# Performance work log

Measured on AMD Instinct MI355X. Metric: run time of the kernel, lower is better.

The kernel has to match this reference:

```python
import jax, jax.numpy as jnp
import numpy as np

N_NODES = 20000
NUM_DRUGS = 2048
NUM_DPI = 200000
IN_C = 256
EMB = 256
HID = 512
OUT = 1
N_CL = 8
B = 16384


def setup_inputs() -> dict:
    key = jax.random.key(0)
    ks = jax.random.split(key, 10)
    x = jax.random.normal(ks[0], (N_NODES, IN_C), jnp.float32)
    # bipartite DPI edges: drug ids in [0, NUM_DRUGS), protein ids in [NUM_DRUGS, N_NODES)
    d = jax.random.randint(ks[1], (NUM_DPI,), 0, NUM_DRUGS)
    p = jax.random.randint(ks[2], (NUM_DPI,), NUM_DRUGS, N_NODES)
    edge_index = jnp.concatenate([jnp.stack([d, p]), jnp.stack([p, d])], axis=1)  # [2, 2*NUM_DPI]
    drug_drug_batch = jax.random.randint(ks[3], (2, B), 0, NUM_DRUGS)
    edge_cell_lines = jax.random.randint(ks[4], (B,), 0, N_CL)
    Wg1 = jax.random.normal(ks[5], (IN_C, EMB), jnp.float32) / np.float32(np.sqrt(IN_C))
    bg1 = jnp.zeros((EMB,), jnp.float32)
    Wg2 = jax.random.normal(ks[6], (EMB, EMB), jnp.float32) / np.float32(np.sqrt(EMB))
    bg2 = jnp.zeros((EMB,), jnp.float32)
    W1 = jax.random.normal(ks[7], (N_CL, 2 * EMB, HID), jnp.float32) / np.float32(np.sqrt(2 * EMB))
    b1 = jnp.zeros((N_CL, HID), jnp.float32)
    W2 = jax.random.normal(ks[8], (N_CL, HID, OUT), jnp.float32) / np.float32(np.sqrt(HID))
    b2 = jnp.zeros((N_CL, OUT), jnp.float32)
    return dict(x=x, edge_index=edge_index, drug_drug_batch=drug_drug_batch,
                edge_cell_lines=edge_cell_lines, num_drugs=NUM_DRUGS,
                Wg1=Wg1, bg1=bg1, Wg2=Wg2, bg2=bg2, W1=W1, b1=b1, W2=W2, b2=b2)


def _gcn(h_in, row, col, W, b, n):
    # PyG GCNConv: self-loops already appended to (row, col); symmetric normalization.
    h = h_in @ W  # [N, EMB]
    deg = jax.ops.segment_sum(jnp.ones(col.shape[0], h.dtype), col, num_segments=n)
    dinv = jnp.where(deg > 0, jax.lax.rsqrt(jnp.maximum(deg, 1e-12)), 0.0)
    msg = h[row] * (dinv[row] * dinv[col])[:, None]
    return jax.ops.segment_sum(msg, col, num_segments=n) + b


def reference(x, edge_index, drug_drug_batch, edge_cell_lines, num_drugs,
              Wg1, bg1, Wg2, bg2, W1, b1, W2, b2):
    n = x.shape[0]
    ar = jnp.arange(n, dtype=edge_index.dtype)
    row = jnp.concatenate([edge_index[0], ar])
    col = jnp.concatenate([edge_index[1], ar])
    h = jax.nn.relu(_gcn(x, row, col, Wg1, bg1, n))
    h = jax.nn.relu(_gcn(h, row, col, Wg2, bg2, n))
    # scatter-mean pool node embeddings of proteins into per-drug graph embeddings
    num_dpi = edge_index.shape[1] // 2
    avg = jnp.sort(edge_index[:, :num_dpi], axis=0)  # row0=drug id, row1=protein id
    node_emb = h[avg[1]]  # [NUM_DPI, EMB]
    sums = jax.ops.segment_sum(node_emb, avg[0], num_segments=num_drugs)
    cnt = jax.ops.segment_sum(jnp.ones(num_dpi, h.dtype), avg[0], num_segments=num_drugs)
    graph = sums / jnp.maximum(cnt, 1.0)[:, None]  # [NUM_DRUGS, EMB]
    xcat = jnp.concatenate([graph[drug_drug_batch[0]], graph[drug_drug_batch[1]]], axis=1)  # [B, 2*EMB]
    # per-cell-line MLP routing: run each expert over all rows, then gather per-row expert output
    n_cl = W1.shape[0]
    outs = jnp.stack([jax.nn.relu(xcat @ W1[c] + b1[c]) @ W2[c] + b2[c] for c in range(n_cl)])  # [C, B, OUT]
    preds = outs[edge_cell_lines, jnp.arange(xcat.shape[0])]  # [B, OUT]
    return preds
```

## Files before the change

### kernel.cpp

```cpp
#include <hip/hip_runtime.h>
#include <hip/hip_bf16.h>

#define N_NODES 20000
#define NUM_DRUGS 2048
#define N_PROT (N_NODES - NUM_DRUGS)
#define NUM_DPI 200000
#define E2 400000
#define CDIM 256
#define HID 512
#define N_CL 8
#define BATCH 16384
#define HN 8192

#define STRD 32
#define STRP 16
#define ELLD 192
#define ELLP 48

#define NB_T64 512
#define NB_TWG 32
#define NB_ZERO 79
#define NB_SPLIT 20000

#define MT_NODE 313

#define NB_AGG_D NUM_DRUGS
#define NB_AGG_P ((N_PROT + 3) / 4)

typedef __attribute__((ext_vector_type(8))) short short8;
typedef __attribute__((ext_vector_type(4))) float floatx4;

__device__ inline unsigned short f2bf(float f) {
    unsigned u = __float_as_uint(f);
    u += 0x7fff + ((u >> 16) & 1);
    return (unsigned short)(u >> 16);
}
__device__ inline float bf2f(unsigned short h) {
    return __uint_as_float((unsigned)h << 16);
}
__device__ inline void split2(float v, unsigned short& h, unsigned short& l) {
    h = f2bf(v);
    l = f2bf(v - bf2f(h));
}
__device__ inline void gload16(const void* g, void* l) {
    __builtin_amdgcn_global_load_lds(
        (const __attribute__((address_space(1))) void*)g,
        (__attribute__((address_space(3))) void*)l, 16, 0, 0);
}
__device__ inline float4 f4fma(float4 v, float s, float4 a) {
    a.x = fmaf(v.x, s, a.x); a.y = fmaf(v.y, s, a.y);
    a.z = fmaf(v.z, s, a.z); a.w = fmaf(v.w, s, a.w);
    return a;
}
__device__ inline float4 bf4(const unsigned short* p) {
    ushort4 q = *(const ushort4*)p;
    return make_float4(bf2f(q.x), bf2f(q.y), bf2f(q.z), bf2f(q.w));
}

__global__ __launch_bounds__(256) void prep_all(
        const float* __restrict__ x, unsigned short* __restrict__ xhi,
        unsigned short* __restrict__ xlo,
        const float* __restrict__ Wg1, const float* __restrict__ Wg2,
        unsigned short* __restrict__ wg1Th, unsigned short* __restrict__ wg1Tl,
        unsigned short* __restrict__ wg2Th, unsigned short* __restrict__ wg2Tl,
        const float* __restrict__ W1, unsigned short* __restrict__ W1Th,
        unsigned short* __restrict__ W1Tl,
        int* __restrict__ cur_d, int* __restrict__ cur_p) {
    __shared__ float ld[64 * 65];
    int b = blockIdx.x;
    int t = threadIdx.x;
    int tx = t & 63, ty = t >> 6;
    if (b < NB_T64) {
        int m = b >> 5;
        int k0 = (b & 3) * 64, n0 = ((b >> 2) & 7) * 64;
        const float* Wm = W1 + (size_t)m * CDIM * HID;
#pragma unroll
        for (int rr = 0; rr < 16; rr++) {
            int kl = rr * 4 + ty;
            ld[tx * 65 + kl] = Wm[(size_t)(k0 + kl) * HID + n0 + tx];
        }
        __syncthreads();
        size_t obase = (size_t)m * HID * CDIM;
#pragma unroll
        for (int rr = 0; rr < 16; rr++) {
            int nl = rr * 4 + ty;
            float v = ld[nl * 65 + tx];
            unsigned short h, l;
            split2(v, h, l);
            size_t o = obase + (size_t)(n0 + nl) * CDIM + k0 + tx;
            W1Th[o] = h;
            W1Tl[o] = l;
        }
        return;
    }
    b -= NB_T64;
    if (b < NB_TWG) {
        const float* W = (b >> 4) ? Wg2 : Wg1;
        unsigned short* hi = (b >> 4) ? wg2Th : wg1Th;
        unsigned short* lo = (b >> 4) ? wg2Tl : wg1Tl;
        int k0 = (b & 3) * 64, n0 = ((b >> 2) & 3) * 64;
#pragma unroll
        for (int rr = 0; rr < 16; rr++) {
            int kl = rr * 4 + ty;
            ld[tx * 65 + kl] = W[(size_t)(k0 + kl) * CDIM + n0 + tx];
        }
        __syncthreads();
#pragma unroll
        for (int rr = 0; rr < 16; rr++) {
            int nl = rr * 4 + ty;
            float v = ld[nl * 65 + tx];
            unsigned short h, l;
            split2(v, h, l);
            size_t o = (size_t)(n0 + nl) * CDIM + k0 + tx;
            hi[o] = h;
            lo[o] = l;
        }
        return;
    }
    b -= NB_TWG;
    if (b < NB_ZERO) {
        int i = b * 256 + t;
        if (i < N_NODES) cur_p[i * STRP] = 0;
        if (i < NUM_DRUGS) cur_d[i * STRD] = 0;
        return;
    }
    b -= NB_ZERO;
    {
        int i = b * 256 + t;
        unsigned short h, l;
        split2(x[i], h, l);
        xhi[i] = h;
        xlo[i] = l;
    }
}

__global__ void fill_ell(const int* __restrict__ ei, int* cur_d, int* adj_drug,
                         int* cur_p, int* adj_prot) {
    int e = blockIdx.x * blockDim.x + threadIdx.x;
    if (e >= NUM_DPI) return;
    int d = ei[e];
    int p = ei[E2 + e];
    int posd = atomicAdd(&cur_d[d * STRD], 1);
    int posp = atomicAdd(&cur_p[p * STRP], 1);
    if (posd < ELLD) adj_drug[d * ELLD + posd] = p;
    if (posp < ELLP) adj_prot[(size_t)p * ELLP + posp] = d;
}

template <int BM, int SWZ>
__global__ __launch_bounds__(256) void gemm_mfma(
        const unsigned short* __restrict__ Ahi, const unsigned short* __restrict__ Alo,
        const unsigned short* __restrict__ BThi, const unsigned short* __restrict__ BTlo,
        float* __restrict__ C, unsigned short* __restrict__ Cbf,
        int M, int K, int N, int mTiles,
        const int* __restrict__ cur_d, const int* __restrict__ cur_p,
        float* __restrict__ dinv) {
    if ((int)blockIdx.x >= mTiles) {
        int i = (((int)blockIdx.x - mTiles) * (int)gridDim.y + (int)blockIdx.y) * 256
                + (int)threadIdx.x;
        if (i < N_NODES) {
            int deg = (i < NUM_DRUGS) ? cur_d[i * STRD] : cur_p[i * STRP];
            dinv[i] = rsqrtf((float)(deg + 1));
        }
        return;
    }
    constexpr int MI = BM / 32;
    __shared__ unsigned short sAh[2][BM * 32], sAl[2][BM * 32];
    __shared__ unsigned short sBh[2][4096], sBl[2][4096];
    int t = threadIdx.x;
    int wv = t >> 6, lane = t & 63, quad = lane >> 4, l15 = lane & 15;
    int bx = blockIdx.x, by = blockIdx.y;
    if constexpr (SWZ) {
        int w = by * 16 + bx;
        bx = (w >> 3) & 15;
        by = ((w >> 7) << 3) | (w & 7);
    }
    int m0 = bx * BM, n0 = by * 128;
    int m0w = (wv >> 1) * (BM / 2), n0w = (wv & 1) * 64;
    floatx4 zero = {0.f, 0.f, 0.f, 0.f};
    floatx4 acc[MI][4];
#pragma unroll
    for (int i = 0; i < MI; i++)
#pragma unroll
        for (int j = 0; j < 4; j++) acc[i][j] = zero;

    auto STAGE = [&](int buf, int kk) {
#pragma unroll
        for (int s = t; s < BM * 4; s += 256) {
            int row = s >> 2, pos = s & 3;
            int ch = pos ^ ((row >> 1) & 3);
            int arow = m0 + row; if (arow > M - 1) arow = M - 1;
            size_t aoff = (size_t)arow * K + kk + ch * 8;
            gload16(Ahi + aoff, &sAh[buf][s * 8]);
            gload16(Alo + aoff, &sAl[buf][s * 8]);
        }
#pragma unroll
        for (int s = t; s < 512; s += 256) {
            int row = s >> 2, pos = s & 3;
            int ch = pos ^ ((row >> 1) & 3);
            int brow = n0 + row; if (brow > N - 1) brow = N - 1;
            size_t boff = (size_t)brow * K + kk + ch * 8;
            gload16(BThi + boff, &sBh[buf][s * 8]);
            gload16(BTlo + boff, &sBl[buf][s * 8]);
        }
    };

    int nk = K >> 5;
    STAGE(0, 0);
    asm volatile("s_waitcnt vmcnt(0)" ::: "memory");
    __builtin_amdgcn_s_barrier();
    int cur = 0;
    for (int it = 0; it < nk; ++it) {
        if (it + 1 < nk) STAGE(cur ^ 1, (it + 1) << 5);
        short8 ah[MI], al[MI], bh[4], bl[4];
        int posq = quad ^ ((l15 >> 1) & 3);
#pragma unroll
        for (int i = 0; i < MI; i++) {
            int sl = (m0w + i * 16 + l15) * 4 + posq;
            ah[i] = *(const short8*)&sAh[cur][sl * 8];
            al[i] = *(const short8*)&sAl[cur][sl * 8];
        }
#pragma unroll
        for (int j = 0; j < 4; j++) {
            int sl = (n0w + j * 16 + l15) * 4 + posq;
            bh[j] = *(const short8*)&sBh[cur][sl * 8];
            bl[j] = *(const short8*)&sBl[cur][sl * 8];
        }
#pragma unroll
        for (int i = 0; i < MI; i++)
#pragma unroll
            for (int j = 0; j < 4; j++) {
                acc[i][j] = __builtin_amdgcn_mfma_f32_16x16x32_bf16(ah[i], bh[j], acc[i][j], 0, 0, 0);
                acc[i][j] = __builtin_amdgcn_mfma_f32_16x16x32_bf16(ah[i], bl[j], acc[i][j], 0, 0, 0);
                acc[i][j] = __builtin_amdgcn_mfma_f32_16x16x32_bf16(al[i], bh[j], acc[i][j], 0, 0, 0);
            }
        if (it + 1 < nk) {
            asm volatile("s_waitcnt vmcnt(0)" ::: "memory");
            __builtin_amdgcn_s_barrier();
            cur ^= 1;
        }
    }
#pragma unroll
    for (int i = 0; i < MI; i++) {
        int gr = m0 + m0w + i * 16 + quad * 4;
#pragma unroll
        for (int r = 0; r < 4; r++) {
            if (gr + r < M) {
#pragma unroll
                for (int j = 0; j < 4; j++) {
                    size_t o = (size_t)(gr + r) * N + n0 + n0w + j * 16 + l15;
                    float v = acc[i][j][r];
                    if (C) C[o] = v;
                    if (Cbf) Cbf[o] = f2bf(v);
                }
            }
        }
    }
}

__global__ __launch_bounds__(256) void aggregate1(const float* __restrict__ tmp,
                                                  const unsigned short* __restrict__ tmpbf,
                                                  const int* __restrict__ cur_d,
                                                  const int* __restrict__ adj_drug,
                                                  const int* __restrict__ cur_p,
                                                  const int* __restrict__ adj_prot,
                                                  const float* __restrict__ dinv,
                                                  const float* __restrict__ bias,
                                                  unsigned short* __restrict__ outhi,
                                                  unsigned short* __restrict__ outlo) {
    __shared__ float4 red[4][64];
    int b = blockIdx.x;
    int lane = threadIdx.x & 63;
    if (b < NB_AGG_D) {
        int d = b;
        int w = threadIdx.x >> 6;
        const int* adj = adj_drug + (size_t)d * ELLD;
        int ecnt = cur_d[d * STRD];
        int e = ecnt < ELLD ? ecnt : ELLD;
        float4 a0 = make_float4(0.f, 0.f, 0.f, 0.f);
        float4 a1 = a0, a2 = a0, a3 = a0;
        int idx = w;
        for (; idx + 12 < e; idx += 16) {
            int j0 = adj[idx], j1 = adj[idx + 4], j2 = adj[idx + 8], j3 = adj[idx + 12];
            float d0 = dinv[j0], d1 = dinv[j1], d2 = dinv[j2], d3 = dinv[j3];
            float4 v0 = bf4(&tmpbf[(size_t)j0 * CDIM + lane * 4]);
            float4 v1 = bf4(&tmpbf[(size_t)j1 * CDIM + lane * 4]);
            float4 v2 = bf4(&tmpbf[(size_t)j2 * CDIM + lane * 4]);
            float4 v3 = bf4(&tmpbf[(size_t)j3 * CDIM + lane * 4]);
            a0 = f4fma(v0, d0, a0);
            a1 = f4fma(v1, d1, a1);
            a2 = f4fma(v2, d2, a2);
            a3 = f4fma(v3, d3, a3);
        }
        for (; idx < e; idx += 4) {
            int j = adj[idx];
            a0 = f4fma(bf4(&tmpbf[(size_t)j * CDIM + lane * 4]), dinv[j], a0);
        }
        a0.x = (a0.x + a1.x) + (a2.x + a3.x);
        a0.y = (a0.y + a1.y) + (a2.y + a3.y);
        a0.z = (a0.z + a1.z) + (a2.z + a3.z);
        a0.w = (a0.w + a1.w) + (a2.w + a3.w);
        red[w][lane] = a0;
        __syncthreads();
        if (w == 0) {
            float di = dinv[d];
            float4 r0 = red[0][lane], r1 = red[1][lane], r2 = red[2][lane], r3 = red[3][lane];
            float4 self = ((const float4*)(tmp + (size_t)d * CDIM))[lane];
            float4 acc;
            acc.x = (r0.x + r1.x) + (r2.x + r3.x) + self.x * di;
            acc.y = (r0.y + r1.y) + (r2.y + r3.y) + self.y * di;
            acc.z = (r0.z + r1.z) + (r2.z + r3.z) + self.z * di;
            acc.w = (r0.w + r1.w) + (r2.w + r3.w) + self.w * di;
            float4 bv = ((const float4*)bias)[lane];
            float4 r;
            r.x = fmaxf(fmaf(acc.x, di, bv.x), 0.f);
            r.y = fmaxf(fmaf(acc.y, di, bv.y), 0.f);
            r.z = fmaxf(fmaf(acc.z, di, bv.z), 0.f);
            r.w = fmaxf(fmaf(acc.w, di, bv.w), 0.f);
            ushort4 h, l;
            split2(r.x, h.x, l.x); split2(r.y, h.y, l.y);
            split2(r.z, h.z, l.z); split2(r.w, h.w, l.w);
            *(ushort4*)&outhi[(size_t)d * CDIM + lane * 4] = h;
            *(ushort4*)&outlo[(size_t)d * CDIM + lane * 4] = l;
        }
        return;
    }
    int i = NUM_DRUGS + (b - NB_AGG_D) * 4 + (threadIdx.x >> 6);
    if (i >= N_NODES) return;
    float di = dinv[i];
    float4 a0 = make_float4(0.f, 0.f, 0.f, 0.f);
    float4 a1 = a0, a2 = a0, a3 = a0;
    const int* adj = adj_prot + (size_t)i * ELLP;
    int e = cur_p[i * STRP];
    int idx = 0;
    for (; idx + 4 <= e; idx += 4) {
        int j0 = adj[idx + 0], j1 = adj[idx + 1];
        int j2 = adj[idx + 2], j3 = adj[idx + 3];
        float d0 = dinv[j0], d1 = dinv[j1], d2 = dinv[j2], d3 = dinv[j3];
        float4 v0 = ((const float4*)(tmp + (size_t)j0 * CDIM))[lane];
        float4 v1 = ((const float4*)(tmp + (size_t)j1 * CDIM))[lane];
        float4 v2 = ((const float4*)(tmp + (size_t)j2 * CDIM))[lane];
        float4 v3 = ((const float4*)(tmp + (size_t)j3 * CDIM))[lane];
        a0 = f4fma(v0, d0, a0);
        a1 = f4fma(v1, d1, a1);
        a2 = f4fma(v2, d2, a2);
        a3 = f4fma(v3, d3, a3);
    }
    for (; idx < e; idx++) {
        int j = adj[idx];
        a0 = f4fma(((const float4*)(tmp + (size_t)j * CDIM))[lane], dinv[j], a0);
    }
    float4 self = ((const float4*)(tmp + (size_t)i * CDIM))[lane];
    float4 acc;
    acc.x = (a0.x + a1.x) + (a2.x + a3.x) + self.x * di;
    acc.y = (a0.y + a1.y) + (a2.y + a3.y) + self.y * di;
    acc.z = (a0.z + a1.z) + (a2.z + a3.z) + self.z * di;
    acc.w = (a0.w + a1.w) + (a2.w + a3.w) + self.w * di;
    float4 bv = ((const float4*)bias)[lane];
    float4 r;
    r.x = fmaxf(fmaf(acc.x, di, bv.x), 0.f);
    r.y = fmaxf(fmaf(acc.y, di, bv.y), 0.f);
    r.z = fmaxf(fmaf(acc.z, di, bv.z), 0.f);
    r.w = fmaxf(fmaf(acc.w, di, bv.w), 0.f);
    ushort4 h, l;
    split2(r.x, h.x, l.x); split2(r.y, h.y, l.y);
    split2(r.z, h.z, l.z); split2(r.w, h.w, l.w);
    *(ushort4*)&outhi[(size_t)i * CDIM + lane * 4] = h;
    *(ushort4*)&outlo[(size_t)i * CDIM + lane * 4] = l;
}

__global__ __launch_bounds__(256) void aggregate2p(const float* __restrict__ tmp2,
                                                   const int* __restrict__ cur_p,
                                                   const int* __restrict__ adj_prot,
                                                   const float* __restrict__ dinv,
                                                   const float* __restrict__ bias,
                                                   unsigned short* __restrict__ h2bf) {
    int w = (blockIdx.x * blockDim.x + threadIdx.x) >> 6;
    int lane = threadIdx.x & 63;
    if (w >= N_PROT) return;
    int i = NUM_DRUGS + w;
    float di = dinv[i];
    float4 a0 = make_float4(0.f, 0.f, 0.f, 0.f);
    float4 a1 = a0, a2 = a0, a3 = a0;
    const int* adj = adj_prot + (size_t)i * ELLP;
    int e = cur_p[i * STRP];
    int idx = 0;
    for (; idx + 4 <= e; idx += 4) {
        int j0 = adj[idx + 0], j1 = adj[idx + 1];
        int j2 = adj[idx + 2], j3 = adj[idx + 3];
        float d0 = dinv[j0], d1 = dinv[j1], d2 = dinv[j2], d3 = dinv[j3];
        float4 v0 = ((const float4*)(tmp2 + (size_t)j0 * CDIM))[lane];
        float4 v1 = ((const float4*)(tmp2 + (size_t)j1 * CDIM))[lane];
        float4 v2 = ((const float4*)(tmp2 + (size_t)j2 * CDIM))[lane];
        float4 v3 = ((const float4*)(tmp2 + (size_t)j3 * CDIM))[lane];
        a0 = f4fma(v0, d0, a0);
        a1 = f4fma(v1, d1, a1);
        a2 = f4fma(v2, d2, a2);
        a3 = f4fma(v3, d3, a3);
    }
    for (; idx < e; idx++) {
        int j = adj[idx];
        a0 = f4fma(((const float4*)(tmp2 + (size_t)j * CDIM))[lane], dinv[j], a0);
    }
    float4 self = ((const float4*)(tmp2 + (size_t)i * CDIM))[lane];
    float4 acc;
    acc.x = (a0.x + a1.x) + (a2.x + a3.x) + self.x * di;
    acc.y = (a0.y + a1.y) + (a2.y + a3.y) + self.y * di;
    acc.z = (a0.z + a1.z) + (a2.z + a3.z) + self.z * di;
    acc.w = (a0.w + a1.w) + (a2.w + a3.w) + self.w * di;
    float4 bv = ((const float4*)bias)[lane];
    ushort4 o;
    o.x = f2bf(fmaxf(fmaf(acc.x, di, bv.x), 0.f));
    o.y = f2bf(fmaxf(fmaf(acc.y, di, bv.y), 0.f));
    o.z = f2bf(fmaxf(fmaf(acc.z, di, bv.z), 0.f));
    o.w = f2bf(fmaxf(fmaf(acc.w, di, bv.w), 0.f));
    *(ushort4*)&h2bf[(size_t)i * CDIM + lane * 4] = o;
}

__global__ __launch_bounds__(256) void pool_drugs(const unsigned short* __restrict__ h2bf,
                                                  unsigned short* __restrict__ Ghi,
                                                  unsigned short* __restrict__ Glo,
                                                  const int* __restrict__ cur_d,
                                                  const int* __restrict__ adj_drug) {
    __shared__ float4 red[4][64];
    int d = blockIdx.x;
    int w = threadIdx.x >> 6, lane = threadIdx.x & 63;
    const int* adj = adj_drug + (size_t)d * ELLD;
    int ecnt = cur_d[d * STRD];
    int e = ecnt < ELLD ? ecnt : ELLD;
    float4 a0 = make_float4(0.f, 0.f, 0.f, 0.f);
    float4 a1 = a0, a2 = a0, a3 = a0;
    int idx = w;
    for (; idx + 12 < e; idx += 16) {
        int j0 = adj[idx], j1 = adj[idx + 4], j2 = adj[idx + 8], j3 = adj[idx + 12];
        float4 v0 = bf4(&h2bf[(size_t)j0 * CDIM + lane * 4]);
        float4 v1 = bf4(&h2bf[(size_t)j1 * CDIM + lane * 4]);
        float4 v2 = bf4(&h2bf[(size_t)j2 * CDIM + lane * 4]);
        float4 v3 = bf4(&h2bf[(size_t)j3 * CDIM + lane * 4]);
        a0.x += v0.x; a0.y += v0.y; a0.z += v0.z; a0.w += v0.w;
        a1.x += v1.x; a1.y += v1.y; a1.z += v1.z; a1.w += v1.w;
        a2.x += v2.x; a2.y += v2.y; a2.z += v2.z; a2.w += v2.w;
        a3.x += v3.x; a3.y += v3.y; a3.z += v3.z; a3.w += v3.w;
    }
    for (; idx < e; idx += 4) {
        float4 v = bf4(&h2bf[(size_t)adj[idx] * CDIM + lane * 4]);
        a0.x += v.x; a0.y += v.y; a0.z += v.z; a0.w += v.w;
    }
    a0.x = (a0.x + a1.x) + (a2.x + a3.x);
    a0.y = (a0.y + a1.y) + (a2.y + a3.y);
    a0.z = (a0.z + a1.z) + (a2.z + a3.z);
    a0.w = (a0.w + a1.w) + (a2.w + a3.w);
    red[w][lane] = a0;
    __syncthreads();
    if (w == 0) {
        float4 r0 = red[0][lane], r1 = red[1][lane], r2 = red[2][lane], r3 = red[3][lane];
        float4 acc;
        acc.x = (r0.x + r1.x) + (r2.x + r3.x);
        acc.y = (r0.y + r1.y) + (r2.y + r3.y);
        acc.z = (r0.z + r1.z) + (r2.z + r3.z);
        acc.w = (r0.w + r1.w) + (r2.w + r3.w);
        float sc = 1.f / (float)(ecnt > 1 ? ecnt : 1);
        acc.x *= sc; acc.y *= sc; acc.z *= sc; acc.w *= sc;
        ushort4 h, l;
        split2(acc.x, h.x, l.x); split2(acc.y, h.y, l.y);
        split2(acc.z, h.z, l.z); split2(acc.w, h.w, l.w);
        *(ushort4*)&Ghi[(size_t)d * CDIM + lane * 4] = h;
        *(ushort4*)&Glo[(size_t)d * CDIM + lane * 4] = l;
    }
}

__global__ __launch_bounds__(256) void mlp_out(const unsigned short* __restrict__ Hbf,
                                               const int* __restrict__ ddb,
                                               const int* __restrict__ ecl,
                                               const float* __restrict__ b1,
                                               const float* __restrict__ W2,
                                               const float* __restrict__ b2,
                                               float* __restrict__ outp) {
    int r = (blockIdx.x * blockDim.x + threadIdx.x) >> 6;
    int lane = threadIdx.x & 63;
    if (r >= BATCH) return;
    int c = ecl[r];
    int d0 = ddb[r], d1 = ddb[BATCH + r];
    int n = lane * 8;
    const unsigned short* h0 = Hbf + (size_t)d0 * HN + (size_t)(c * 2) * HID + n;
    const unsigned short* h1 = Hbf + (size_t)d1 * HN + (size_t)(c * 2 + 1) * HID + n;
    const float* b1e = b1 + (size_t)c * HID + n;
    const float* w2e = W2 + (size_t)c * HID + n;
    short8 a8 = *(const short8*)h0;
    short8 b8 = *(const short8*)h1;
    float4 bb0 = *(const float4*)(b1e);
    float4 bb1 = *(const float4*)(b1e + 4);
    float4 w0 = *(const float4*)(w2e);
    float4 w1 = *(const float4*)(w2e + 4);
    float s = 0.f;
    float h;
    h = bf2f((unsigned short)a8[0]) + bf2f((unsigned short)b8[0]) + bb0.x;
    s = fmaf(fmaxf(h, 0.f), w0.x, s);
    h = bf2f((unsigned short)a8[1]) + bf2f((unsigned short)b8[1]) + bb0.y;
    s = fmaf(fmaxf(h, 0.f), w0.y, s);
    h = bf2f((unsigned short)a8[2]) + bf2f((unsigned short)b8[2]) + bb0.z;
    s = fmaf(fmaxf(h, 0.f), w0.z, s);
    h = bf2f((unsigned short)a8[3]) + bf2f((unsigned short)b8[3]) + bb0.w;
    s = fmaf(fmaxf(h, 0.f), w0.w, s);
    h = bf2f((unsigned short)a8[4]) + bf2f((unsigned short)b8[4]) + bb1.x;
    s = fmaf(fmaxf(h, 0.f), w1.x, s);
    h = bf2f((unsigned short)a8[5]) + bf2f((unsigned short)b8[5]) + bb1.y;
    s = fmaf(fmaxf(h, 0.f), w1.y, s);
    h = bf2f((unsigned short)a8[6]) + bf2f((unsigned short)b8[6]) + bb1.z;
    s = fmaf(fmaxf(h, 0.f), w1.z, s);
    h = bf2f((unsigned short)a8[7]) + bf2f((unsigned short)b8[7]) + bb1.w;
    s = fmaf(fmaxf(h, 0.f), w1.w, s);
    s += __shfl_xor(s, 1);
    s += __shfl_xor(s, 2);
    s += __shfl_xor(s, 4);
    s += __shfl_xor(s, 8);
    s += __shfl_xor(s, 16);
    s += __shfl_xor(s, 32);
    if (lane == 0) outp[r] = s + b2[c];
}

extern "C" void kernel_launch(void* const* d_in, const int* in_sizes, int n_in,
                              void* d_out, int out_size, void* d_ws, size_t ws_size,
                              hipStream_t stream) {
    const float* x   = (const float*)d_in[0];
    const int* ei    = (const int*)d_in[1];
    const int* ddb   = (const int*)d_in[2];
    const int* ecl   = (const int*)d_in[3];
    const float* Wg1 = (const float*)d_in[5];
    const float* bg1 = (const float*)d_in[6];
    const float* Wg2 = (const float*)d_in[7];
    const float* bg2 = (const float*)d_in[8];
    const float* W1  = (const float*)d_in[9];
    const float* b1  = (const float*)d_in[10];
    const float* W2  = (const float*)d_in[11];
    const float* b2  = (const float*)d_in[12];
    float* outp = (float*)d_out;

    const size_t NC = (size_t)N_NODES * CDIM;
    const size_t HRES = (size_t)NUM_DRUGS * HN * sizeof(float);
    char* r0 = (char*)d_ws;
    unsigned short* Hbf   = (unsigned short*)d_ws;
    float* tmp            = (float*)r0;
    unsigned short* t1bf  = (unsigned short*)(r0 + 20480000);
    unsigned short* h2bf  = t1bf;
    unsigned short* h1hi  = (unsigned short*)(r0 + 30720000);
    unsigned short* h1lo  = (unsigned short*)(r0 + 40960000);
    unsigned short* xhi   = h1hi;
    unsigned short* xlo   = h1lo;
    char* p = r0 + 51200000;
    auto alloc = [&](size_t bytes) {
        char* r = p;
        p += (bytes + 255) & ~size_t(255);
        return (void*)r;
    };
    float* dinv    = (float*)alloc(sizeof(float) * N_NODES);
    int* cur_d     = (int*)alloc(sizeof(int) * NUM_DRUGS * STRD);
    int* cur_p     = (int*)alloc(sizeof(int) * N_NODES * STRP);
    int* adj_drug  = (int*)alloc(sizeof(int) * NUM_DRUGS * ELLD);
    int* adj_prot  = (int*)alloc(sizeof(int) * (size_t)N_NODES * ELLP);
    p = (char*)d_ws + ((HRES + 255) & ~size_t(255));
    unsigned short* Ghi   = (unsigned short*)alloc(2 * NUM_DRUGS * CDIM);
    unsigned short* Glo   = (unsigned short*)alloc(2 * NUM_DRUGS * CDIM);
    unsigned short* wg1Th = (unsigned short*)alloc(2 * CDIM * CDIM);
    unsigned short* wg1Tl = (unsigned short*)alloc(2 * CDIM * CDIM);
    unsigned short* wg2Th = (unsigned short*)alloc(2 * CDIM * CDIM);
    unsigned short* wg2Tl = (unsigned short*)alloc(2 * CDIM * CDIM);
    unsigned short* W1Th  = (unsigned short*)alloc(2 * (size_t)N_CL * HID * HID);
    unsigned short* W1Tl  = (unsigned short*)alloc(2 * (size_t)N_CL * HID * HID);

    prep_all<<<NB_T64 + NB_TWG + NB_ZERO + NB_SPLIT, 256, 0, stream>>>(
        x, xhi, xlo, Wg1, Wg2, wg1Th, wg1Tl, wg2Th, wg2Tl, W1, W1Th, W1Tl,
        cur_d, cur_p);
    fill_ell<<<(NUM_DPI + 255) / 256, 256, 0, stream>>>(ei, cur_d, adj_drug,
                                                        cur_p, adj_prot);
    gemm_mfma<64, 0><<<dim3(MT_NODE + 40, 2), 256, 0, stream>>>(
        xhi, xlo, wg1Th, wg1Tl, tmp, t1bf, N_NODES, CDIM, CDIM,
        MT_NODE, cur_d, cur_p, dinv);
    aggregate1<<<NB_AGG_D + NB_AGG_P, 256, 0, stream>>>(
        tmp, t1bf, cur_d, adj_drug, cur_p, adj_prot, dinv, bg1, h1hi, h1lo);
    gemm_mfma<64, 0><<<dim3(MT_NODE, 2), 256, 0, stream>>>(
        h1hi, h1lo, wg2Th, wg2Tl, tmp, nullptr, N_NODES, CDIM, CDIM,
        MT_NODE, nullptr, nullptr, nullptr);
    aggregate2p<<<(N_PROT * 64 + 255) / 256, 256, 0, stream>>>(
        tmp, cur_p, adj_prot, dinv, bg2, h2bf);
    pool_drugs<<<NUM_DRUGS, 256, 0, stream>>>(h2bf, Ghi, Glo, cur_d, adj_drug);
    gemm_mfma<128, 1><<<dim3(NUM_DRUGS / 128, HN / 128), 256, 0, stream>>>(
        Ghi, Glo, W1Th, W1Tl, nullptr, Hbf, NUM_DRUGS, CDIM, HN,
        NUM_DRUGS / 128, nullptr, nullptr, nullptr);
    mlp_out<<<(BATCH * 64) / 256, 256, 0, stream>>>(Hbf, ddb, ecl, b1, W2, b2, outp);
}
```

Baseline: 251.0 us.

## Add triple-buffered 128x64 MFMA GEMM with XCD-aware tile mapping for drug MLP

Result: slower. 257.9 us (+2.8%).

```diff
diff --git a/kernel.cpp b/kernel.cpp
--- a/kernel.cpp
+++ b/kernel.cpp
@@ -146,7 +146,7 @@
     if (posp < ELLP) adj_prot[(size_t)p * ELLP + posp] = d;
 }
 
-template <int BM, int SWZ>
+template <int BM>
 __global__ __launch_bounds__(256) void gemm_mfma(
         const unsigned short* __restrict__ Ahi, const unsigned short* __restrict__ Alo,
         const unsigned short* __restrict__ BThi, const unsigned short* __restrict__ BTlo,
@@ -169,11 +169,6 @@
     int t = threadIdx.x;
     int wv = t >> 6, lane = t & 63, quad = lane >> 4, l15 = lane & 15;
     int bx = blockIdx.x, by = blockIdx.y;
-    if constexpr (SWZ) {
-        int w = by * 16 + bx;
-        bx = (w >> 3) & 15;
-        by = ((w >> 7) << 3) | (w & 7);
-    }
     int m0 = bx * BM, n0 = by * 128;
     int m0w = (wv >> 1) * (BM / 2), n0w = (wv & 1) * 64;
     floatx4 zero = {0.f, 0.f, 0.f, 0.f};
@@ -252,6 +247,97 @@
                     if (C) C[o] = v;
                     if (Cbf) Cbf[o] = f2bf(v);
                 }
+            }
+        }
+    }
+}
+
+__global__ __launch_bounds__(256) void gemm_ring(
+        const unsigned short* __restrict__ Ahi, const unsigned short* __restrict__ Alo,
+        const unsigned short* __restrict__ BThi, const unsigned short* __restrict__ BTlo,
+        unsigned short* __restrict__ Cbf, int M, int K, int N) {
+    constexpr int BM = 128, BN = 64, MI = 4, NJ = 2;
+    __shared__ unsigned short sAh[3][BM * 32], sAl[3][BM * 32];
+    __shared__ unsigned short sBh[3][BN * 32], sBl[3][BN * 32];
+    int t = threadIdx.x;
+    int wv = t >> 6, lane = t & 63, quad = lane >> 4, l15 = lane & 15;
+    int w = (int)blockIdx.y * 16 + (int)blockIdx.x;
+    int xcd = w & 7, j = w >> 3;
+    int bx = j & 15;
+    int by = xcd * 16 + (j >> 4);
+    int m0 = bx * BM, n0 = by * BN;
+    int m0w = (wv >> 1) * 64, n0w = (wv & 1) * 32;
+    floatx4 zero = {0.f, 0.f, 0.f, 0.f};
+    floatx4 acc[MI][NJ];
+#pragma unroll
+    for (int i = 0; i < MI; i++)
+#pragma unroll
+        for (int jj = 0; jj < NJ; jj++) acc[i][jj] = zero;
+
+    auto STAGE = [&](int buf, int it) {
+        int kk = it << 5;
+#pragma unroll
+        for (int s = t; s < BM * 4; s += 256) {
+            int row = s >> 2, pos = s & 3;
+            int ch = pos ^ ((row >> 1) & 3);
+            size_t aoff = (size_t)(m0 + row) * K + kk + ch * 8;
+            gload16(Ahi + aoff, &sAh[buf][s * 8]);
+            gload16(Alo + aoff, &sAl[buf][s * 8]);
+        }
+        {
+            int s = t;
+            int row = s >> 2, pos = s & 3;
+            int ch = pos ^ ((row >> 1) & 3);
+            size_t boff = (size_t)(n0 + row) * K + kk + ch * 8;
+            gload16(BThi + boff, &sBh[buf][s * 8]);
+            gload16(BTlo + boff, &sBl[buf][s * 8]);
+        }
+    };
+
+    int nk = K >> 5;
+    STAGE(0, 0);
+    if (nk > 1) STAGE(1, 1);
+    for (int it = 0; it < nk; ++it) {
+        if (it + 1 < nk) {
+            asm volatile("s_waitcnt vmcnt(6)" ::: "memory");
+        } else {
+            asm volatile("s_waitcnt vmcnt(0)" ::: "memory");
+        }
+        __builtin_amdgcn_s_barrier();
+        if (it + 2 < nk) STAGE((it + 2) % 3, it + 2);
+        int cur = it % 3;
+        short8 ah[MI], al[MI], bh[NJ], bl[NJ];
+        int posq = quad ^ ((l15 >> 1) & 3);
+#pragma unroll
+        for (int i = 0; i < MI; i++) {
+            int sl = (m0w + i * 16 + l15) * 4 + posq;
+            ah[i] = *(const short8*)&sAh[cur][sl * 8];
+            al[i] = *(const short8*)&sAl[cur][sl * 8];
+        }
+#pragma unroll
+        for (int jj = 0; jj < NJ; jj++) {
+            int sl = (n0w + jj * 16 + l15) * 4 + posq;
+            bh[jj] = *(const short8*)&sBh[cur][sl * 8];
+            bl[jj] = *(const short8*)&sBl[cur][sl * 8];
+        }
+#pragma unroll
+        for (int i = 0; i < MI; i++)
+#pragma unroll
+            for (int jj = 0; jj < NJ; jj++) {
+                acc[i][jj] = __builtin_amdgcn_mfma_f32_16x16x32_bf16(ah[i], bh[jj], acc[i][jj], 0, 0, 0);
+                acc[i][jj] = __builtin_amdgcn_mfma_f32_16x16x32_bf16(ah[i], bl[jj], acc[i][jj], 0, 0, 0);
+                acc[i][jj] = __builtin_amdgcn_mfma_f32_16x16x32_bf16(al[i], bh[jj], acc[i][jj], 0, 0, 0);
+            }
+    }
+#pragma unroll
+    for (int i = 0; i < MI; i++) {
+        int gr = m0 + m0w + i * 16 + quad * 4;
+#pragma unroll
+        for (int r = 0; r < 4; r++) {
+#pragma unroll
+            for (int jj = 0; jj < NJ; jj++) {
+                size_t o = (size_t)(gr + r) * N + n0 + n0w + jj * 16 + l15;
+                Cbf[o] = f2bf(acc[i][jj][r]);
             }
         }
     }
@@ -572,19 +658,18 @@
         cur_d, cur_p);
     fill_ell<<<(NUM_DPI + 255) / 256, 256, 0, stream>>>(ei, cur_d, adj_drug,
                                                         cur_p, adj_prot);
-    gemm_mfma<64, 0><<<dim3(MT_NODE + 40, 2), 256, 0, stream>>>(
+    gemm_mfma<64><<<dim3(MT_NODE + 40, 2), 256, 0, stream>>>(
         xhi, xlo, wg1Th, wg1Tl, tmp, t1bf, N_NODES, CDIM, CDIM,
         MT_NODE, cur_d, cur_p, dinv);
     aggregate1<<<NB_AGG_D + NB_AGG_P, 256, 0, stream>>>(
         tmp, t1bf, cur_d, adj_drug, cur_p, adj_prot, dinv, bg1, h1hi, h1lo);
-    gemm_mfma<64, 0><<<dim3(MT_NODE, 2), 256, 0, stream>>>(
+    gemm_mfma<64><<<dim3(MT_NODE, 2), 256, 0, stream>>>(
         h1hi, h1lo, wg2Th, wg2Tl, tmp, nullptr, N_NODES, CDIM, CDIM,
         MT_NODE, nullptr, nullptr, nullptr);
     aggregate2p<<<(N_PROT * 64 + 255) / 256, 256, 0, stream>>>(
         tmp, cur_p, adj_prot, dinv, bg2, h2bf);
     pool_drugs<<<NUM_DRUGS, 256, 0, stream>>>(h2bf, Ghi, Glo, cur_d, adj_drug);
-    gemm_mfma<128, 1><<<dim3(NUM_DRUGS / 128, HN / 128), 256, 0, stream>>>(
-        Ghi, Glo, W1Th, W1Tl, nullptr, Hbf, NUM_DRUGS, CDIM, HN,
-        NUM_DRUGS / 128, nullptr, nullptr, nullptr);
+    gemm_ring<<<dim3(NUM_DRUGS / 128, HN / 64), 256, 0, stream>>>(
+        Ghi, Glo, W1Th, W1Tl, Hbf, NUM_DRUGS, CDIM, HN);
     mlp_out<<<(BATCH * 64) / 256, 256, 0, stream>>>(Hbf, ddb, ecl, b1, W2, b2, outp);
 }
```
